# Optimization experiments

Hardware: AMD Instinct MI355X
Metric: run time of the kernel (lower is better)

## Reference

```python
import jax, jax.numpy as jnp
import numpy as np

NUM_NODES = 100000
NUM_EDGES = 1600000
IN_DIM = 128
HID = 128
OUT_DIM = 5


def setup_inputs() -> dict:
    key = jax.random.key(0)
    ks = jax.random.split(key, 8)
    x = jax.random.normal(ks[0], (NUM_NODES, IN_DIM), dtype=jnp.float32)
    edges = jax.random.randint(ks[1], (2, NUM_EDGES), 0, NUM_NODES, dtype=jnp.int32)
    s = 1.0 / np.sqrt(IN_DIM)
    W1 = jax.random.uniform(ks[2], (IN_DIM, HID), jnp.float32, -s, s)
    b1 = jax.random.uniform(ks[3], (HID,), jnp.float32, -s, s)
    sh = 1.0 / np.sqrt(HID)
    W2 = jax.random.uniform(ks[4], (HID, HID), jnp.float32, -sh, sh)
    b2 = jax.random.uniform(ks[5], (HID,), jnp.float32, -sh, sh)
    Wp = jax.random.uniform(ks[6], (HID, OUT_DIM), jnp.float32, -sh, sh)
    bp = jax.random.uniform(ks[7], (OUT_DIM,), jnp.float32, -sh, sh)
    return {"x": x, "edges": edges, "W1": W1, "b1": b1, "W2": W2, "b2": b2, "Wp": Wp, "bp": bp}


def _gnn_layer(x, src, tgt, W, b):
    # scatter-add of source features into targets (mean aggregation)
    agg = jax.ops.segment_sum(x[src], tgt, num_segments=NUM_NODES)  # [N, d]
    cnt = jax.ops.segment_sum(jnp.ones_like(tgt, dtype=x.dtype), tgt, num_segments=NUM_NODES)
    cnt = jnp.maximum(cnt, 1.0)  # clamp(min=1)
    agg = agg / cnt[:, None]
    combined = x + agg  # residual
    return jax.nn.relu(combined @ W + b)


def reference(x, edges, W1, b1, W2, b2, Wp, bp):
    src, tgt = edges[0], edges[1]
    h = _gnn_layer(x, src, tgt, W1, b1)
    h = _gnn_layer(h, src, tgt, W2, b2)
    return h @ Wp + bp  # [N, OUT_DIM]
```

## Files before the change

kernel.cpp:

```cpp
#include <hip/hip_runtime.h>

typedef unsigned int uint32;
typedef unsigned short ushort16;

typedef __attribute__((ext_vector_type(8))) short short8;
typedef __attribute__((ext_vector_type(4))) float f32x4;


#define RSH 11
#define NRG 2048
#define CAP 49152
#define CH  2048

__device__ __forceinline__ ushort16 f2bf(float f) {
    uint32 u = __float_as_uint(f);
    u += 0x7fffu + ((u >> 16) & 1u);
    return (ushort16)(u >> 16);
}
__device__ __forceinline__ float bfhi(uint32 u) { return __uint_as_float(u & 0xffff0000u); }
__device__ __forceinline__ float bflo(uint32 u) { return __uint_as_float(u << 16); }
__device__ __forceinline__ uint32 pack2(float a, float b) {
    return (uint32)f2bf(a) | ((uint32)f2bf(b) << 16);
}

union U16 { uint4 u; short8 s; };
__device__ __forceinline__ short8 ld_frag(const ushort16* p) {
    U16 x; x.u = *(const uint4*)p; return x.s;
}

#define ACC8(v) \
    acc[0] += bflo(v.x); acc[1] += bfhi(v.x); \
    acc[2] += bflo(v.y); acc[3] += bfhi(v.y); \
    acc[4] += bflo(v.z); acc[5] += bfhi(v.z); \
    acc[6] += bflo(v.w); acc[7] += bfhi(v.w);

__global__ __launch_bounds__(256)
void count_prep_kernel(const int* __restrict__ tgt, int* __restrict__ hist,
                       const float* __restrict__ W1, const float* __restrict__ W2,
                       ushort16* __restrict__ Wt1, ushort16* __restrict__ Wt2,
                       int E, int PB, int R) {
    int tid = threadIdx.x, blk = blockIdx.x;
    if (blk >= PB) {
        int idx = blk - PB;
        const float* W = (idx >> 3) ? W2 : W1;
        ushort16* Wt = (idx >> 3) ? Wt2 : Wt1;
        int i0 = (idx & 7) * 2048 + tid * 8;
        float4 a = *(const float4*)(W + i0);
        float4 b = *(const float4*)(W + i0 + 4);
        int k = i0 >> 7, col = i0 & 127;
        Wt[(col + 0) * 128 + k] = f2bf(a.x);
        Wt[(col + 1) * 128 + k] = f2bf(a.y);
        Wt[(col + 2) * 128 + k] = f2bf(a.z);
        Wt[(col + 3) * 128 + k] = f2bf(a.w);
        Wt[(col + 4) * 128 + k] = f2bf(b.x);
        Wt[(col + 5) * 128 + k] = f2bf(b.y);
        Wt[(col + 6) * 128 + k] = f2bf(b.z);
        Wt[(col + 7) * 128 + k] = f2bf(b.w);
        return;
    }
    __shared__ int cnt[64];
    if (tid < 64) cnt[tid] = 0;
    __syncthreads();
    int q0 = blk * (CH / 4), q1 = min(q0 + CH / 4, E / 4);
    for (int q = q0 + tid; q < q1; q += 256) {
        int4 t = ((const int4*)tgt)[q];
        atomicAdd(&cnt[t.x >> RSH], 1);
        atomicAdd(&cnt[t.y >> RSH], 1);
        atomicAdd(&cnt[t.z >> RSH], 1);
        atomicAdd(&cnt[t.w >> RSH], 1);
    }
    if (blk == 0 && tid == 0)
        for (int e = (E / 4) * 4; e < E; ++e) atomicAdd(&cnt[tgt[e] >> RSH], 1);
    __syncthreads();
    if (tid < R) hist[(size_t)blk * 64 + tid] = cnt[tid];
}

__global__ __launch_bounds__(256)
void scan_kernel(int* __restrict__ hist, int* __restrict__ total, int PB) {
    __shared__ int sd[256];
    __shared__ int carrySh;
    int r = blockIdx.x, tid = threadIdx.x;
    if (tid == 0) carrySh = 0;
    __syncthreads();
    int chunks = (PB + 255) >> 8;
    for (int ch = 0; ch < chunks; ++ch) {
        int g = ch * 256 + tid;
        int v = (g < PB) ? hist[(size_t)g * 64 + r] : 0;
        int c0 = carrySh;
        sd[tid] = v;
        __syncthreads();
        for (int o = 1; o < 256; o <<= 1) {
            int t = (tid >= o) ? sd[tid - o] : 0;
            __syncthreads();
            sd[tid] += t;
            __syncthreads();
        }
        if (g < PB) hist[(size_t)g * 64 + r] = sd[tid] - v + c0;
        int tot = sd[255];
        __syncthreads();
        if (tid == 0) carrySh = c0 + tot;
        __syncthreads();
    }
    if (tid == 0) total[r] = carrySh;
}

__global__ __launch_bounds__(256)
void scatter_kernel(const int* __restrict__ src, const int* __restrict__ tgt,
                    const int* __restrict__ hist, uint2* __restrict__ rlist,
                    int E, int R) {
    __shared__ int cb[64];
    __shared__ int cnt[64];
    int tid = threadIdx.x, blk = blockIdx.x;
    if (tid < 64) {
        cnt[tid] = 0;
        cb[tid] = (tid < R) ? hist[(size_t)blk * 64 + tid] : 0;
    }
    __syncthreads();
    int q0 = blk * (CH / 4), q1 = min(q0 + CH / 4, E / 4);
    for (int q = q0 + tid; q < q1; q += 256) {
        int4 t = ((const int4*)tgt)[q];
        int4 s = ((const int4*)src)[q];
        int r0 = t.x >> RSH, r1 = t.y >> RSH, r2 = t.z >> RSH, r3 = t.w >> RSH;
        int p0 = cb[r0] + atomicAdd(&cnt[r0], 1);
        int p1 = cb[r1] + atomicAdd(&cnt[r1], 1);
        int p2 = cb[r2] + atomicAdd(&cnt[r2], 1);
        int p3 = cb[r3] + atomicAdd(&cnt[r3], 1);
        if (p0 < CAP) rlist[(size_t)r0 * CAP + p0] = make_uint2((uint32)s.x, (uint32)t.x);
        if (p1 < CAP) rlist[(size_t)r1 * CAP + p1] = make_uint2((uint32)s.y, (uint32)t.y);
        if (p2 < CAP) rlist[(size_t)r2 * CAP + p2] = make_uint2((uint32)s.z, (uint32)t.z);
        if (p3 < CAP) rlist[(size_t)r3 * CAP + p3] = make_uint2((uint32)s.w, (uint32)t.w);
    }
    if (blk == 0 && tid == 0) {
        for (int e = (E / 4) * 4; e < E; ++e) {
            int t = tgt[e], r = t >> RSH;
            int p = cb[r] + atomicAdd(&cnt[r], 1);
            if (p < CAP) rlist[(size_t)r * CAP + p] = make_uint2((uint32)src[e], (uint32)t);
        }
    }
}

template<int MODE>
__device__ __forceinline__
void gemm_rows(const void* __restrict__ Asrc, const ushort16* __restrict__ Wt,
               const float* __restrict__ bias, int M,
               ushort16* __restrict__ outB, int r0w) {
    const int lane = threadIdx.x & 63;
    const int l15 = lane & 15;
    const int quad = lane >> 4;

    int arow = r0w + l15;
    if (arow >= M) arow = M - 1;

    short8 afr[4];
    if (MODE == 1) {
        const float* ap = (const float*)Asrc + (size_t)arow * 128 + quad * 8;
#pragma unroll
        for (int kt = 0; kt < 4; ++kt) {
            float4 a0 = *(const float4*)(ap + kt * 32);
            float4 a1 = *(const float4*)(ap + kt * 32 + 4);
            short8 f;
            f[0] = (short)f2bf(a0.x); f[1] = (short)f2bf(a0.y);
            f[2] = (short)f2bf(a0.z); f[3] = (short)f2bf(a0.w);
            f[4] = (short)f2bf(a1.x); f[5] = (short)f2bf(a1.y);
            f[6] = (short)f2bf(a1.z); f[7] = (short)f2bf(a1.w);
            afr[kt] = f;
        }
    } else if (MODE == 2) {
        const ushort16* aptr = (const ushort16*)Asrc + (size_t)arow * 128 + quad * 8;
#pragma unroll
        for (int kt = 0; kt < 4; ++kt) {
            uint4 v = *(const uint4*)(aptr + kt * 32);
            const float* bb = bias + kt * 32 + quad * 8;
            float4 b0 = *(const float4*)bb;
            float4 b1 = *(const float4*)(bb + 4);
            uint32 w0 = pack2(fmaxf(bflo(v.x) + b0.x, 0.f), fmaxf(bfhi(v.x) + b0.y, 0.f));
            uint32 w1 = pack2(fmaxf(bflo(v.y) + b0.z, 0.f), fmaxf(bfhi(v.y) + b0.w, 0.f));
            uint32 w2 = pack2(fmaxf(bflo(v.z) + b1.x, 0.f), fmaxf(bfhi(v.z) + b1.y, 0.f));
            uint32 w3 = pack2(fmaxf(bflo(v.w) + b1.z, 0.f), fmaxf(bfhi(v.w) + b1.w, 0.f));
            U16 u; u.u = make_uint4(w0, w1, w2, w3);
            afr[kt] = u.s;
        }
    } else {
        const ushort16* aptr = (const ushort16*)Asrc + (size_t)arow * 128 + quad * 8;
#pragma unroll
        for (int kt = 0; kt < 4; ++kt) afr[kt] = ld_frag(aptr + kt * 32);
    }

    f32x4 acc[8];
#pragma unroll
    for (int t = 0; t < 8; ++t) acc[t] = (f32x4){0.f, 0.f, 0.f, 0.f};

#pragma unroll
    for (int t = 0; t < 8; ++t) {
        const ushort16* bptr = Wt + (size_t)(16 * t + l15) * 128 + quad * 8;
        short8 b0 = ld_frag(bptr);
        short8 b1 = ld_frag(bptr + 32);
        short8 b2 = ld_frag(bptr + 64);
        short8 b3 = ld_frag(bptr + 96);
        acc[t] = __builtin_amdgcn_mfma_f32_16x16x32_bf16(afr[0], b0, acc[t], 0, 0, 0);
        acc[t] = __builtin_amdgcn_mfma_f32_16x16x32_bf16(afr[1], b1, acc[t], 0, 0, 0);
        acc[t] = __builtin_amdgcn_mfma_f32_16x16x32_bf16(afr[2], b2, acc[t], 0, 0, 0);
        acc[t] = __builtin_amdgcn_mfma_f32_16x16x32_bf16(afr[3], b3, acc[t], 0, 0, 0);
    }

#pragma unroll
    for (int t = 0; t < 8; ++t) {
        float ov[4];
        ov[0] = acc[t].x; ov[1] = acc[t].y; ov[2] = acc[t].z; ov[3] = acc[t].w;
#pragma unroll
        for (int r = 0; r < 4; ++r) {
            float nb = __shfl_xor(ov[r], 1, 64);
            int row = r0w + quad * 4 + r;
            if (((l15 & 1) == 0) && row < M) {
                *(uint32*)(outB + (size_t)row * 128 + 16 * t + l15) = pack2(ov[r], nb);
            }
        }
    }
}

__global__ __launch_bounds__(1024)
void csr_gemm1_kernel(const uint2* __restrict__ rlist, const int* __restrict__ total,
                      int* __restrict__ start, int* __restrict__ deg,
                      int* __restrict__ csr, int N, int R,
                      const float* __restrict__ x, const ushort16* __restrict__ Wt1,
                      ushort16* __restrict__ ybuf) {
    int blk = blockIdx.x;
    int tid = threadIdx.x;
    if (blk >= R) {
        int gid = blk - R;
        gemm_rows<1>(x, Wt1, nullptr, N, ybuf, gid * 256 + (tid >> 6) * 16);
        return;
    }
    __shared__ int hist[NRG];
    __shared__ int sd[1024];
    __shared__ int carrySh;
    __shared__ int rbaseSh, countSh;

    int r = blk;
    if (tid == 0) countSh = min(total[r], CAP);
    if (tid < 64) {
        int v = (tid < R) ? total[tid] : 0;
        int pm = (tid < r) ? v : 0;
#pragma unroll
        for (int o = 1; o < 64; o <<= 1) pm += __shfl_xor(pm, o, 64);
        if (tid == 0) rbaseSh = pm;
    }
    for (int i = tid; i < NRG; i += 1024) hist[i] = 0;
    __syncthreads();
    int count = countSh;
    const uint2* rl = rlist + (size_t)r * CAP;
    int n0 = r << RSH;

    {
        int i = tid;
        for (; i + 3072 < count; i += 4096) {
            uint2 a = rl[i], b = rl[i + 1024], c = rl[i + 2048], d = rl[i + 3072];
            atomicAdd(&hist[a.y & (NRG - 1)], 1);
            atomicAdd(&hist[b.y & (NRG - 1)], 1);
            atomicAdd(&hist[c.y & (NRG - 1)], 1);
            atomicAdd(&hist[d.y & (NRG - 1)], 1);
        }
        for (; i < count; i += 1024)
            atomicAdd(&hist[rl[i].y & (NRG - 1)], 1);
    }
    __syncthreads();

    if (tid == 0) carrySh = rbaseSh;
    __syncthreads();
    for (int ch = 0; ch < 2; ++ch) {
        int idx = ch * 1024 + tid;
        int v = hist[idx];
        int c0 = carrySh;
        sd[tid] = v;
        __syncthreads();
        for (int o = 1; o < 1024; o <<= 1) {
            int t = (tid >= o) ? sd[tid - o] : 0;
            __syncthreads();
            sd[tid] += t;
            __syncthreads();
        }
        int excl = sd[tid] - v + c0;
        int tot = sd[1023];
        int node = n0 + idx;
        if (node < N) { start[node] = excl; deg[node] = v; }
        __syncthreads();
        hist[idx] = excl;
        if (tid == 0) carrySh = c0 + tot;
        __syncthreads();
    }

    {
        int i = tid;
        for (; i + 3072 < count; i += 4096) {
            uint2 a = rl[i], b = rl[i + 1024], c = rl[i + 2048], d = rl[i + 3072];
            int pa = atomicAdd(&hist[a.y & (NRG - 1)], 1);
            int pb = atomicAdd(&hist[b.y & (NRG - 1)], 1);
            int pc = atomicAdd(&hist[c.y & (NRG - 1)], 1);
            int pd = atomicAdd(&hist[d.y & (NRG - 1)], 1);
            csr[pa] = (int)a.x;
            csr[pb] = (int)b.x;
            csr[pc] = (int)c.x;
            csr[pd] = (int)d.x;
        }
        for (; i < count; i += 1024) {
            uint2 e = rl[i];
            int p = atomicAdd(&hist[e.y & (NRG - 1)], 1);
            csr[p] = (int)e.x;
        }
    }
}

__global__ __launch_bounds__(256)
void gemm_biasrelu_kernel(const ushort16* __restrict__ A, const ushort16* __restrict__ Wt,
                          const float* __restrict__ bias, int M,
                          ushort16* __restrict__ outB) {
    gemm_rows<2>(A, Wt, bias, M, outB, blockIdx.x * 64 + ((threadIdx.x >> 6)) * 16);
}

__global__ __launch_bounds__(256, 4)
void agg_combine_bf16_kernel(const ushort16* __restrict__ hb,
                             const int* __restrict__ startv, const int* __restrict__ degv,
                             const int* __restrict__ csr,
                             uint32* __restrict__ outb, int N) {
    int wid = (blockIdx.x * 256 + threadIdx.x) >> 6;
    int lane = threadIdx.x & 63;
    if (wid >= N) return;
    int g = lane >> 4, sl = lane & 15;
    int s0 = startv[wid];
    int deg = degv[wid];
    int fi = sl * 4 + g;
    uint32 su = ((const uint32*)hb)[(size_t)wid * 64 + fi];

    float acc[8];
#pragma unroll
    for (int j = 0; j < 8; ++j) acc[j] = 0.f;

    int base = 0;
    for (; base + 8 <= deg; base += 8) {
        int i0 = csr[s0 + base + g];
        int i1 = csr[s0 + base + 4 + g];
        uint4 v0 = *(const uint4*)(hb + (size_t)i0 * 128 + sl * 8);
        uint4 v1 = *(const uint4*)(hb + (size_t)i1 * 128 + sl * 8);
        ACC8(v0); ACC8(v1);
    }
    for (; base < deg; base += 4) {
        int e = base + g;
        if (e < deg) {
            int s = csr[s0 + e];
            uint4 v = *(const uint4*)(hb + (size_t)s * 128 + sl * 8);
            ACC8(v);
        }
    }
#pragma unroll
    for (int j = 0; j < 8; ++j) {
        acc[j] += __shfl_xor(acc[j], 16, 64);
        acc[j] += __shfl_xor(acc[j], 32, 64);
    }
    float inv = 1.f / fmaxf((float)deg, 1.f);
    float ax = (g == 0) ? acc[0] : (g == 1) ? acc[2] : (g == 2) ? acc[4] : acc[6];
    float ay = (g == 0) ? acc[1] : (g == 1) ? acc[3] : (g == 2) ? acc[5] : acc[7];
    outb[(size_t)wid * 64 + fi] = pack2(bflo(su) + ax * inv, bfhi(su) + ay * inv);
}

__global__ __launch_bounds__(256)
void proj_kernel(const ushort16* __restrict__ w, const float* __restrict__ b2,
                 const float* __restrict__ Wp, const float* __restrict__ bp,
                 float* __restrict__ out, int N) {
    __shared__ float wps[640];
    __shared__ float b2s[128];
    int tid = threadIdx.x;
    for (int i = tid; i < 640; i += 256) wps[i] = Wp[i];
    if (tid < 128) b2s[tid] = b2[tid];
    __syncthreads();
    int n = blockIdx.x * 256 + tid;
    if (n >= N) return;
    const uint4* row = (const uint4*)(w + (size_t)n * 128);
    float p0 = 0.f, p1 = 0.f, p2 = 0.f, p3 = 0.f, p4 = 0.f;
#pragma unroll
    for (int q = 0; q < 16; ++q) {
        uint4 v = row[q];
        int c = q * 8;
        uint32 ww[4] = {v.x, v.y, v.z, v.w};
#pragma unroll
        for (int k = 0; k < 4; ++k) {
            float hlo = fmaxf(bflo(ww[k]) + b2s[c + 2 * k],     0.f);
            float hhi = fmaxf(bfhi(ww[k]) + b2s[c + 2 * k + 1], 0.f);
            const float* wl = &wps[(c + 2 * k) * 5];
            p0 += hlo * wl[0] + hhi * wl[5];
            p1 += hlo * wl[1] + hhi * wl[6];
            p2 += hlo * wl[2] + hhi * wl[7];
            p3 += hlo * wl[3] + hhi * wl[8];
            p4 += hlo * wl[4] + hhi * wl[9];
        }
    }
    float* o = out + (size_t)n * 5;
    o[0] = p0 + bp[0];
    o[1] = p1 + bp[1];
    o[2] = p2 + bp[2];
    o[3] = p3 + bp[3];
    o[4] = p4 + bp[4];
}

extern "C" void kernel_launch(void* const* d_in, const int* in_sizes, int n_in,
                              void* d_out, int out_size, void* d_ws, size_t ws_size,
                              hipStream_t stream) {
    const float* x     = (const float*)d_in[0];
    const int*   edges = (const int*)d_in[1];
    const float* W1    = (const float*)d_in[2];
    const float* b1    = (const float*)d_in[3];
    const float* W2    = (const float*)d_in[4];
    const float* b2    = (const float*)d_in[5];
    const float* Wp    = (const float*)d_in[6];
    const float* bp    = (const float*)d_in[7];
    float* out = (float*)d_out;

    int N = in_sizes[0] / 128;
    int E = in_sizes[1] / 2;
    const int* src = edges;
    const int* tgt = edges + E;

    const int R  = (N + NRG - 1) >> RSH;
    const int PB = (E + CH - 1) / CH;

    char* ws = (char*)d_ws;
    size_t off = 0;
    auto alloc = [&](size_t bytes) {
        char* p = ws + off;
        off = (off + bytes + 255) & ~(size_t)255;
        return p;
    };
    int*      deg     = (int*)alloc((size_t)N * 4);
    int*      start   = (int*)alloc((size_t)N * 4);
    int*      csr     = (int*)alloc((size_t)E * 4);
    int*      hist    = (int*)alloc((size_t)PB * 64 * 4);
    int*      total   = (int*)alloc(64 * 4);
    ushort16* ybuf    = (ushort16*)alloc((size_t)N * 128 * 2);
    ushort16* abuf    = (ushort16*)alloc((size_t)N * 128 * 2);
    ushort16* Wt1     = (ushort16*)alloc(128 * 128 * 2);
    ushort16* Wt2     = (ushort16*)alloc(128 * 128 * 2);
    uint2*    rlist   = (uint2*)alloc((size_t)R * CAP * 8);
    (void)ws_size;

    const int g1Blocks   = (N + 255) / 256;
    const int gemmBlocks = (N + 63) / 64;
    const int aggBlocks  = (N + 3) / 4;
    const int projBlocks = (N + 255) / 256;

    count_prep_kernel<<<PB + 16, 256, 0, stream>>>(tgt, hist, W1, W2, Wt1, Wt2,
                                                   E, PB, R);
    scan_kernel<<<R, 256, 0, stream>>>(hist, total, PB);
    scatter_kernel<<<PB, 256, 0, stream>>>(src, tgt, hist, rlist, E, R);
    csr_gemm1_kernel<<<R + g1Blocks, 1024, 0, stream>>>(rlist, total, start, deg,
                                                        csr, N, R, x, Wt1, ybuf);
    agg_combine_bf16_kernel<<<aggBlocks, 256, 0, stream>>>(ybuf, start, deg, csr,
                                                           (uint32*)abuf, N);
    gemm_biasrelu_kernel<<<gemmBlocks, 256, 0, stream>>>(abuf, Wt2, b1, N, ybuf);
    agg_combine_bf16_kernel<<<aggBlocks, 256, 0, stream>>>(ybuf, start, deg, csr,
                                                           (uint32*)abuf, N);
    proj_kernel<<<projBlocks, 256, 0, stream>>>(abuf, b2, Wp, bp, out, N);
}
```

Before: 329.6 us.

## Compute node degrees with global atomics and allocate CSR offsets via atomic bump

```diff
diff --git a/kernel.cpp b/kernel.cpp
--- a/kernel.cpp
+++ b/kernel.cpp
@@ -35,10 +35,11 @@
     acc[6] += bflo(v.w); acc[7] += bfhi(v.w);
 
 __global__ __launch_bounds__(256)
-void count_prep_kernel(const int* __restrict__ tgt, int* __restrict__ hist,
-                       const float* __restrict__ W1, const float* __restrict__ W2,
-                       ushort16* __restrict__ Wt1, ushort16* __restrict__ Wt2,
-                       int E, int PB, int R) {
+void count_deg_prep_kernel(const int* __restrict__ tgt, int* __restrict__ hist,
+                           int* __restrict__ deg, int* __restrict__ gcur,
+                           const float* __restrict__ W1, const float* __restrict__ W2,
+                           ushort16* __restrict__ Wt1, ushort16* __restrict__ Wt2,
+                           int E, int PB, int R) {
     int tid = threadIdx.x, blk = blockIdx.x;
     if (blk >= PB) {
         int idx = blk - PB;
@@ -58,6 +59,7 @@
         Wt[(col + 7) * 128 + k] = f2bf(b.w);
         return;
     }
+    if (blk == 0 && tid == 0) *gcur = 0;
     __shared__ int cnt[64];
     if (tid < 64) cnt[tid] = 0;
     __syncthreads();
@@ -68,18 +70,46 @@
         atomicAdd(&cnt[t.y >> RSH], 1);
         atomicAdd(&cnt[t.z >> RSH], 1);
         atomicAdd(&cnt[t.w >> RSH], 1);
-    }
-    if (blk == 0 && tid == 0)
-        for (int e = (E / 4) * 4; e < E; ++e) atomicAdd(&cnt[tgt[e] >> RSH], 1);
+        atomicAdd(&deg[t.x], 1);
+        atomicAdd(&deg[t.y], 1);
+        atomicAdd(&deg[t.z], 1);
+        atomicAdd(&deg[t.w], 1);
+    }
+    if (blk == 0 && tid == 0) {
+        for (int e = (E / 4) * 4; e < E; ++e) {
+            atomicAdd(&cnt[tgt[e] >> RSH], 1);
+            atomicAdd(&deg[tgt[e]], 1);
+        }
+    }
     __syncthreads();
     if (tid < R) hist[(size_t)blk * 64 + tid] = cnt[tid];
 }
 
 __global__ __launch_bounds__(256)
-void scan_kernel(int* __restrict__ hist, int* __restrict__ total, int PB) {
+void alloc_scan_kernel(const int* __restrict__ deg, int* __restrict__ start,
+                       int* __restrict__ gcur, int N, int AB,
+                       int* __restrict__ hist, int* __restrict__ total, int PB) {
+    int tid = threadIdx.x, blk = blockIdx.x;
+    if (blk < AB) {
+        int i = blk * 256 + tid;
+        int lane = tid & 63;
+        int d = (i < N) ? deg[i] : 0;
+        int incl = d;
+#pragma unroll
+        for (int o = 1; o < 64; o <<= 1) {
+            int t = __shfl_up(incl, o, 64);
+            if (lane >= o) incl += t;
+        }
+        int wtotal = __shfl(incl, 63, 64);
+        int base = 0;
+        if (lane == 63) base = atomicAdd(gcur, wtotal);
+        base = __shfl(base, 63, 64);
+        if (i < N) start[i] = base + incl - d;
+        return;
+    }
     __shared__ int sd[256];
     __shared__ int carrySh;
-    int r = blockIdx.x, tid = threadIdx.x;
+    int r = blk - AB;
     if (tid == 0) carrySh = 0;
     __syncthreads();
     int chunks = (PB + 255) >> 8;
@@ -220,8 +250,8 @@
 
 __global__ __launch_bounds__(1024)
 void csr_gemm1_kernel(const uint2* __restrict__ rlist, const int* __restrict__ total,
-                      int* __restrict__ start, int* __restrict__ deg,
-                      int* __restrict__ csr, int N, int R,
+                      const int* __restrict__ start, int* __restrict__ csr,
+                      int N, int R,
                       const float* __restrict__ x, const ushort16* __restrict__ Wt1,
                       ushort16* __restrict__ ybuf) {
     int blk = blockIdx.x;
@@ -231,82 +261,35 @@
         gemm_rows<1>(x, Wt1, nullptr, N, ybuf, gid * 256 + (tid >> 6) * 16);
         return;
     }
-    __shared__ int hist[NRG];
-    __shared__ int sd[1024];
-    __shared__ int carrySh;
-    __shared__ int rbaseSh, countSh;
-
+    __shared__ int cur[NRG];
+    __shared__ int countSh;
     int r = blk;
     if (tid == 0) countSh = min(total[r], CAP);
-    if (tid < 64) {
-        int v = (tid < R) ? total[tid] : 0;
-        int pm = (tid < r) ? v : 0;
-#pragma unroll
-        for (int o = 1; o < 64; o <<= 1) pm += __shfl_xor(pm, o, 64);
-        if (tid == 0) rbaseSh = pm;
-    }
-    for (int i = tid; i < NRG; i += 1024) hist[i] = 0;
+    int n0 = r << RSH;
+    for (int i = tid; i < NRG; i += 1024) {
+        int node = n0 + i;
+        cur[i] = (node < N) ? start[node] : 0;
+    }
     __syncthreads();
     int count = countSh;
     const uint2* rl = rlist + (size_t)r * CAP;
-    int n0 = r << RSH;
-
-    {
-        int i = tid;
-        for (; i + 3072 < count; i += 4096) {
-            uint2 a = rl[i], b = rl[i + 1024], c = rl[i + 2048], d = rl[i + 3072];
-            atomicAdd(&hist[a.y & (NRG - 1)], 1);
-            atomicAdd(&hist[b.y & (NRG - 1)], 1);
-            atomicAdd(&hist[c.y & (NRG - 1)], 1);
-            atomicAdd(&hist[d.y & (NRG - 1)], 1);
-        }
-        for (; i < count; i += 1024)
-            atomicAdd(&hist[rl[i].y & (NRG - 1)], 1);
-    }
-    __syncthreads();
-
-    if (tid == 0) carrySh = rbaseSh;
-    __syncthreads();
-    for (int ch = 0; ch < 2; ++ch) {
-        int idx = ch * 1024 + tid;
-        int v = hist[idx];
-        int c0 = carrySh;
-        sd[tid] = v;
-        __syncthreads();
-        for (int o = 1; o < 1024; o <<= 1) {
-            int t = (tid >= o) ? sd[tid - o] : 0;
-            __syncthreads();
-            sd[tid] += t;
-            __syncthreads();
-        }
-        int excl = sd[tid] - v + c0;
-        int tot = sd[1023];
-        int node = n0 + idx;
-        if (node < N) { start[node] = excl; deg[node] = v; }
-        __syncthreads();
-        hist[idx] = excl;
-        if (tid == 0) carrySh = c0 + tot;
-        __syncthreads();
-    }
-
-    {
-        int i = tid;
-        for (; i + 3072 < count; i += 4096) {
-            uint2 a = rl[i], b = rl[i + 1024], c = rl[i + 2048], d = rl[i + 3072];
-            int pa = atomicAdd(&hist[a.y & (NRG - 1)], 1);
-            int pb = atomicAdd(&hist[b.y & (NRG - 1)], 1);
-            int pc = atomicAdd(&hist[c.y & (NRG - 1)], 1);
-            int pd = atomicAdd(&hist[d.y & (NRG - 1)], 1);
-            csr[pa] = (int)a.x;
-            csr[pb] = (int)b.x;
-            csr[pc] = (int)c.x;
-            csr[pd] = (int)d.x;
-        }
-        for (; i < count; i += 1024) {
-            uint2 e = rl[i];
-            int p = atomicAdd(&hist[e.y & (NRG - 1)], 1);
-            csr[p] = (int)e.x;
-        }
+
+    int i = tid;
+    for (; i + 3072 < count; i += 4096) {
+        uint2 a = rl[i], b = rl[i + 1024], c = rl[i + 2048], d = rl[i + 3072];
+        int pa = atomicAdd(&cur[a.y & (NRG - 1)], 1);
+        int pb = atomicAdd(&cur[b.y & (NRG - 1)], 1);
+        int pc = atomicAdd(&cur[c.y & (NRG - 1)], 1);
+        int pd = atomicAdd(&cur[d.y & (NRG - 1)], 1);
+        csr[pa] = (int)a.x;
+        csr[pb] = (int)b.x;
+        csr[pc] = (int)c.x;
+        csr[pd] = (int)d.x;
+    }
+    for (; i < count; i += 1024) {
+        uint2 e = rl[i];
+        int p = atomicAdd(&cur[e.y & (NRG - 1)], 1);
+        csr[p] = (int)e.x;
     }
 }
 
@@ -421,6 +404,7 @@
 
     const int R  = (N + NRG - 1) >> RSH;
     const int PB = (E + CH - 1) / CH;
+    const int AB = (N + 255) / 256;
 
     char* ws = (char*)d_ws;
     size_t off = 0;
@@ -429,7 +413,7 @@
         off = (off + bytes + 255) & ~(size_t)255;
         return p;
     };
-    int*      deg     = (int*)alloc((size_t)N * 4);
+    int*      deg     = (int*)alloc((size_t)(N + 1) * 4);
     int*      start   = (int*)alloc((size_t)N * 4);
     int*      csr     = (int*)alloc((size_t)E * 4);
     int*      hist    = (int*)alloc((size_t)PB * 64 * 4);
@@ -439,6 +423,7 @@
     ushort16* Wt1     = (ushort16*)alloc(128 * 128 * 2);
     ushort16* Wt2     = (ushort16*)alloc(128 * 128 * 2);
     uint2*    rlist   = (uint2*)alloc((size_t)R * CAP * 8);
+    int*      gcur    = deg + N;
     (void)ws_size;
 
     const int g1Blocks   = (N + 255) / 256;
@@ -446,11 +431,13 @@
     const int aggBlocks  = (N + 3) / 4;
     const int projBlocks = (N + 255) / 256;
 
-    count_prep_kernel<<<PB + 16, 256, 0, stream>>>(tgt, hist, W1, W2, Wt1, Wt2,
-                                                   E, PB, R);
-    scan_kernel<<<R, 256, 0, stream>>>(hist, total, PB);
+    (void)hipMemsetAsync(deg, 0, (size_t)N * 4, stream);
+    count_deg_prep_kernel<<<PB + 16, 256, 0, stream>>>(tgt, hist, deg, gcur,
+                                                       W1, W2, Wt1, Wt2, E, PB, R);
+    alloc_scan_kernel<<<AB + R, 256, 0, stream>>>(deg, start, gcur, N, AB,
+                                                  hist, total, PB);
     scatter_kernel<<<PB, 256, 0, stream>>>(src, tgt, hist, rlist, E, R);
-    csr_gemm1_kernel<<<R + g1Blocks, 1024, 0, stream>>>(rlist, total, start, deg,
+    csr_gemm1_kernel<<<R + g1Blocks, 1024, 0, stream>>>(rlist, total, start,
                                                         csr, N, R, x, Wt1, ybuf);
     agg_combine_bf16_kernel<<<aggBlocks, 256, 0, stream>>>(ybuf, start, deg, csr,
                                                            (uint32*)abuf, N);
```

After: 413.1 us. 25.3% more time.
